# Kernel tuning notes

Measured on AMD Instinct MI355X. Metric: run time of the kernel, lower is better.

## Reference

```python
import jax, jax.numpy as jnp
import numpy as np
from jax import lax

GAMMA = 5.0
BETA = -2.5
EPS_EDGE = 1e-6
EPS_STD = 1e-6


def _fixed_kernels():
    """Stack 3 Sobel-x, 3 Sobel-y and Laplacian kernels, zero-padded to 7x7.
    Zero-padding a kernel symmetrically + padding=3 conv is mathematically
    identical to the per-scale padding=scale//2 convs in the original.
    Channel order: gx3, gy3, gx5, gy5, gx7, gy7, lap."""
    s3 = np.array([[-1, 0, 1], [-2, 0, 2], [-1, 0, 1]], np.float32)
    s5 = np.array([[-1, -2, 0, 2, 1], [-4, -8, 0, 8, 4], [-6, -12, 0, 12, 6],
                   [-4, -8, 0, 8, 4], [-1, -2, 0, 2, 1]], np.float32)
    s7 = np.array([[-1, -4, -5, 0, 5, 4, 1], [-6, -24, -30, 0, 30, 24, 6],
                   [-15, -60, -75, 0, 75, 60, 15], [-20, -80, -100, 0, 100, 80, 20],
                   [-15, -60, -75, 0, 75, 60, 15], [-6, -24, -30, 0, 30, 24, 6],
                   [-1, -4, -5, 0, 5, 4, 1]], np.float32)
    lap = np.array([[0, 1, 0], [1, -4, 1], [0, 1, 0]], np.float32)
    ks = []
    for k in (s3, s3.T, s5, s5.T, s7, s7.T, lap):
        p = (7 - k.shape[0]) // 2
        ks.append(np.pad(k, p))
    return jnp.asarray(np.stack(ks)[:, None])  # [7,1,7,7] OIHW


_KERNELS = _fixed_kernels()


def setup_inputs() -> dict:
    key = jax.random.key(0)
    x = jax.random.normal(key, (16, 64, 256, 256), dtype=jnp.float32)
    return {"x": x}


def reference(x):
    # grayscale: mean over channels -> [B,1,H,W]
    x_gray = x.mean(axis=1, keepdims=True)
    # single grouped conv producing all 7 filtered maps: [B,7,H,W]
    g = lax.conv_general_dilated(
        x_gray, _KERNELS.astype(x.dtype), window_strides=(1, 1),
        padding=((3, 3), (3, 3)),
        dimension_numbers=("NCHW", "OIHW", "NCHW"))
    gx = g[:, 0:6:2]  # [B,3,H,W]
    gy = g[:, 1:6:2]  # [B,3,H,W]
    edges = jnp.sqrt(gx * gx + gy * gy + EPS_EDGE)      # [B,3,H,W]
    lap_edge = jnp.abs(g[:, 6:7])                        # [B,1,H,W]
    # mean over the 4 concatenated edge channels
    combined = (edges.sum(axis=1, keepdims=True) + lap_edge) / 4.0  # [B,1,H,W]
    # per-image normalization (torch .std is unbiased -> ddof=1)
    mu = combined.mean(axis=(2, 3), keepdims=True)
    sigma = jnp.std(combined, axis=(2, 3), keepdims=True, ddof=1) + EPS_STD
    normalized = (combined - mu) / sigma
    boundary_map = jax.nn.sigmoid(GAMMA * normalized + BETA)
    return x * (1.0 + boundary_map)
```

## Files before the change

kernel.cpp:

```cpp
#include <hip/hip_runtime.h>
#include <math.h>

#define N_IMG 16
#define CCH   64
#define H     256
#define W     256
#define HW    (H*W)
#define HW4   (HW/4)
#define TS    16

typedef float fx4 __attribute__((ext_vector_type(4)));

__global__ __launch_bounds__(256) void gray_kernel(const float4* __restrict__ x,
                                                   float4* __restrict__ gray) {
    int bid = blockIdx.x;
    int n   = bid >> 6;
    int p4  = ((bid & 63) << 8) + threadIdx.x;
    const float4* xp = x + (size_t)n * CCH * HW4 + p4;
    float4 a0 = make_float4(0.f, 0.f, 0.f, 0.f);
    float4 a1 = a0, a2 = a0, a3 = a0;
    #pragma unroll
    for (int c = 0; c < CCH; c += 4) {
        float4 v0 = xp[(size_t)(c + 0) * HW4];
        float4 v1 = xp[(size_t)(c + 1) * HW4];
        float4 v2 = xp[(size_t)(c + 2) * HW4];
        float4 v3 = xp[(size_t)(c + 3) * HW4];
        a0.x += v0.x; a0.y += v0.y; a0.z += v0.z; a0.w += v0.w;
        a1.x += v1.x; a1.y += v1.y; a1.z += v1.z; a1.w += v1.w;
        a2.x += v2.x; a2.y += v2.y; a2.z += v2.z; a2.w += v2.w;
        a3.x += v3.x; a3.y += v3.y; a3.z += v3.z; a3.w += v3.w;
    }
    const float s = 1.0f / 64.0f;
    float4 acc;
    acc.x = (a0.x + a1.x + a2.x + a3.x) * s;
    acc.y = (a0.y + a1.y + a2.y + a3.y) * s;
    acc.z = (a0.z + a1.z + a2.z + a3.z) * s;
    acc.w = (a0.w + a1.w + a2.w + a3.w) * s;
    gray[(size_t)n * HW4 + p4] = acc;
}

__global__ __launch_bounds__(256) void conv_kernel(const float* __restrict__ gray,
                                                   float* __restrict__ comb,
                                                   float2* __restrict__ part) {
    __shared__ float t[TS + 6][TS + 7];
    __shared__ float rs[256];
    __shared__ float rq[256];
    int n  = blockIdx.z;
    int h0 = blockIdx.y * TS - 3;
    int w0 = blockIdx.x * TS - 3;
    const float* g = gray + (size_t)n * HW;

    int tid = threadIdx.y * TS + threadIdx.x;
    for (int i = tid; i < 22 * 22; i += 256) {
        int r  = i / 22, c2 = i - r * 22;
        int hh = h0 + r, ww = w0 + c2;
        t[r][c2] = (hh >= 0 && hh < H && ww >= 0 && ww < W) ? g[hh * W + ww] : 0.f;
    }
    __syncthreads();

    int ty = threadIdx.y, tx = threadIdx.x;
    float v[7][7];
    #pragma unroll
    for (int i = 0; i < 7; ++i)
        #pragma unroll
        for (int j = 0; j < 7; ++j)
            v[i][j] = t[ty + i][tx + j];

    float gx7 = 0.f, gy7 = 0.f;
    {
        const float vw[7] = {1.f, 6.f, 15.f, 20.f, 15.f, 6.f, 1.f};
        const float dw[7] = {-1.f, -4.f, -5.f, 0.f, 5.f, 4.f, 1.f};
        #pragma unroll
        for (int i = 0; i < 7; ++i) {
            float rh  = -v[i][0] - 4.f*v[i][1] - 5.f*v[i][2] + 5.f*v[i][4] + 4.f*v[i][5] + v[i][6];
            float rsu =  v[i][0] + 6.f*v[i][1] + 15.f*v[i][2] + 20.f*v[i][3] + 15.f*v[i][4] + 6.f*v[i][5] + v[i][6];
            gx7 += vw[i] * rh;
            gy7 += dw[i] * rsu;
        }
    }
    float gx5 = 0.f, gy5 = 0.f;
    {
        const float vw[5] = {1.f, 4.f, 6.f, 4.f, 1.f};
        const float dw[5] = {-1.f, -2.f, 0.f, 2.f, 1.f};
        #pragma unroll
        for (int i = 0; i < 5; ++i) {
            float rh  = -v[i+1][1] - 2.f*v[i+1][2] + 2.f*v[i+1][4] + v[i+1][5];
            float rsu =  v[i+1][1] + 4.f*v[i+1][2] + 6.f*v[i+1][3] + 4.f*v[i+1][4] + v[i+1][5];
            gx5 += vw[i] * rh;
            gy5 += dw[i] * rsu;
        }
    }
    float gx3 = 0.f, gy3 = 0.f;
    {
        const float vw[3] = {1.f, 2.f, 1.f};
        const float dw[3] = {-1.f, 0.f, 1.f};
        #pragma unroll
        for (int i = 0; i < 3; ++i) {
            float rh  = v[i+2][4] - v[i+2][2];
            float rsu = v[i+2][2] + 2.f*v[i+2][3] + v[i+2][4];
            gx3 += vw[i] * rh;
            gy3 += dw[i] * rsu;
        }
    }
    float lap = v[2][3] + v[4][3] + v[3][2] + v[3][4] - 4.f*v[3][3];

    float e3 = sqrtf(gx3*gx3 + gy3*gy3 + 1e-6f);
    float e5 = sqrtf(gx5*gx5 + gy5*gy5 + 1e-6f);
    float e7 = sqrtf(gx7*gx7 + gy7*gy7 + 1e-6f);
    float combined = (e3 + e5 + e7 + fabsf(lap)) * 0.25f;

    comb[(size_t)n * HW + (size_t)(h0 + 3 + ty) * W + (w0 + 3 + tx)] = combined;

    rs[tid] = combined;
    rq[tid] = combined * combined;
    __syncthreads();
    for (int off = 128; off > 0; off >>= 1) {
        if (tid < off) {
            rs[tid] += rs[tid + off];
            rq[tid] += rq[tid + off];
        }
        __syncthreads();
    }
    if (tid == 0) {
        int blockLin = blockIdx.y * (W / TS) + blockIdx.x;
        part[n * 256 + blockLin] = make_float2(rs[0], rq[0]);
    }
}

__global__ __launch_bounds__(256) void mul_kernel(const float4* __restrict__ x,
                                                  const float4* __restrict__ comb4,
                                                  const float2* __restrict__ part,
                                                  fx4* __restrict__ out) {
    __shared__ float rs[256];
    __shared__ float rq[256];
    int bid  = blockIdx.x;
    int n    = bid >> 7;
    int rest = bid & 127;
    int half = rest >> 6;
    int p4   = ((rest & 63) << 8) + threadIdx.x;
    int tid  = threadIdx.x;

    float2 p = part[n * 256 + tid];
    rs[tid] = p.x;
    rq[tid] = p.y;
    __syncthreads();
    for (int off = 128; off > 0; off >>= 1) {
        if (tid < off) {
            rs[tid] += rs[tid + off];
            rq[tid] += rq[tid + off];
        }
        __syncthreads();
    }
    float mu  = rs[0] / (float)HW;
    float var = (rq[0] - (float)HW * mu * mu) / (float)(HW - 1);
    var = fmaxf(var, 0.f);
    float inv = 1.0f / (sqrtf(var) + 1e-6f);

    float4 c = comb4[((size_t)n << 14) + p4];
    fx4 f;
    f.x = 1.0f + 1.0f / (1.0f + __expf(2.5f - 5.0f * (c.x - mu) * inv));
    f.y = 1.0f + 1.0f / (1.0f + __expf(2.5f - 5.0f * (c.y - mu) * inv));
    f.z = 1.0f + 1.0f / (1.0f + __expf(2.5f - 5.0f * (c.z - mu) * inv));
    f.w = 1.0f + 1.0f / (1.0f + __expf(2.5f - 5.0f * (c.w - mu) * inv));

    const int ch0 = half * 32;
    const float4* xp = x   + (size_t)n * CCH * HW4 + (size_t)ch0 * HW4 + p4;
    fx4*          op = out + (size_t)n * CCH * HW4 + (size_t)ch0 * HW4 + p4;
    #pragma unroll 8
    for (int ch = 0; ch < 32; ++ch) {
        float4 v = xp[(size_t)ch * HW4];
        fx4 r;
        r.x = v.x * f.x;
        r.y = v.y * f.y;
        r.z = v.z * f.z;
        r.w = v.w * f.w;
        __builtin_nontemporal_store(r, &op[(size_t)ch * HW4]);
    }
}

extern "C" void kernel_launch(void* const* d_in, const int* in_sizes, int n_in,
                              void* d_out, int out_size, void* d_ws, size_t ws_size,
                              hipStream_t stream) {
    const float* x = (const float*)d_in[0];
    float* out = (float*)d_out;
    char* ws = (char*)d_ws;

    float*  gray  = (float*)ws;
    float*  comb  = (float*)(ws + (size_t)N_IMG * HW * 4);
    float2* part  = (float2*)(ws + (size_t)2 * N_IMG * HW * 4);

    gray_kernel<<<N_IMG * 64, 256, 0, stream>>>((const float4*)x, (float4*)gray);

    dim3 cgrid(W / TS, H / TS, N_IMG);
    conv_kernel<<<cgrid, dim3(TS, TS), 0, stream>>>(gray, comb, part);

    mul_kernel<<<N_IMG * 128, 256, 0, stream>>>((const float4*)x, (const float4*)comb,
                                                part, (fx4*)out);
}
```

Baseline: 142.0 us.

## Finalize per-image stats in last conv block; split mul into quarter-channel blocks

```diff
diff --git a/kernel.cpp b/kernel.cpp
--- a/kernel.cpp
+++ b/kernel.cpp
@@ -41,10 +41,13 @@
 
 __global__ __launch_bounds__(256) void conv_kernel(const float* __restrict__ gray,
                                                    float* __restrict__ comb,
-                                                   float2* __restrict__ part) {
+                                                   float2* __restrict__ part,
+                                                   float2* __restrict__ stats,
+                                                   unsigned* __restrict__ cnt) {
     __shared__ float t[TS + 6][TS + 7];
     __shared__ float rs[256];
     __shared__ float rq[256];
+    __shared__ int sIsLast;
     int n  = blockIdx.z;
     int h0 = blockIdx.y * TS - 3;
     int w0 = blockIdx.x * TS - 3;
@@ -124,37 +127,45 @@
     if (tid == 0) {
         int blockLin = blockIdx.y * (W / TS) + blockIdx.x;
         part[n * 256 + blockLin] = make_float2(rs[0], rq[0]);
-    }
-}
-
-__global__ __launch_bounds__(256) void mul_kernel(const float4* __restrict__ x,
+        __threadfence();
+        unsigned old = atomicAdd(&cnt[n], 1u);
+        sIsLast = (old == 255u);
+    }
+    __syncthreads();
+
+    if (sIsLast) {
+        __threadfence();
+        float2 p = part[n * 256 + tid];
+        rs[tid] = p.x;
+        rq[tid] = p.y;
+        __syncthreads();
+        for (int off = 128; off > 0; off >>= 1) {
+            if (tid < off) {
+                rs[tid] += rs[tid + off];
+                rq[tid] += rq[tid + off];
+            }
+            __syncthreads();
+        }
+        if (tid == 0) {
+            float mu  = rs[0] / (float)HW;
+            float var = (rq[0] - (float)HW * mu * mu) / (float)(HW - 1);
+            var = fmaxf(var, 0.f);
+            stats[n] = make_float2(mu, 1.0f / (sqrtf(var) + 1e-6f));
+        }
+    }
+}
+
+__global__ __launch_bounds__(256) void mul_kernel(const fx4* __restrict__ x,
                                                   const float4* __restrict__ comb4,
-                                                  const float2* __restrict__ part,
+                                                  const float2* __restrict__ stats,
                                                   fx4* __restrict__ out) {
-    __shared__ float rs[256];
-    __shared__ float rq[256];
-    int bid  = blockIdx.x;
-    int n    = bid >> 7;
-    int rest = bid & 127;
-    int half = rest >> 6;
-    int p4   = ((rest & 63) << 8) + threadIdx.x;
-    int tid  = threadIdx.x;
-
-    float2 p = part[n * 256 + tid];
-    rs[tid] = p.x;
-    rq[tid] = p.y;
-    __syncthreads();
-    for (int off = 128; off > 0; off >>= 1) {
-        if (tid < off) {
-            rs[tid] += rs[tid + off];
-            rq[tid] += rq[tid + off];
-        }
-        __syncthreads();
-    }
-    float mu  = rs[0] / (float)HW;
-    float var = (rq[0] - (float)HW * mu * mu) / (float)(HW - 1);
-    var = fmaxf(var, 0.f);
-    float inv = 1.0f / (sqrtf(var) + 1e-6f);
+    int bid = blockIdx.x;
+    int n   = bid >> 8;
+    int q   = (bid >> 6) & 3;
+    int p4  = ((bid & 63) << 8) + threadIdx.x;
+
+    float2 st = stats[n];
+    float mu = st.x, inv = st.y;
 
     float4 c = comb4[((size_t)n << 14) + p4];
     fx4 f;
@@ -163,17 +174,13 @@
     f.z = 1.0f + 1.0f / (1.0f + __expf(2.5f - 5.0f * (c.z - mu) * inv));
     f.w = 1.0f + 1.0f / (1.0f + __expf(2.5f - 5.0f * (c.w - mu) * inv));
 
-    const int ch0 = half * 32;
-    const float4* xp = x   + (size_t)n * CCH * HW4 + (size_t)ch0 * HW4 + p4;
-    fx4*          op = out + (size_t)n * CCH * HW4 + (size_t)ch0 * HW4 + p4;
-    #pragma unroll 8
-    for (int ch = 0; ch < 32; ++ch) {
-        float4 v = xp[(size_t)ch * HW4];
-        fx4 r;
-        r.x = v.x * f.x;
-        r.y = v.y * f.y;
-        r.z = v.z * f.z;
-        r.w = v.w * f.w;
+    const int ch0 = q * 16;
+    const fx4* xp = x   + (size_t)n * CCH * HW4 + (size_t)ch0 * HW4 + p4;
+    fx4*       op = out + (size_t)n * CCH * HW4 + (size_t)ch0 * HW4 + p4;
+    #pragma unroll
+    for (int ch = 0; ch < 16; ++ch) {
+        fx4 v = __builtin_nontemporal_load(&xp[(size_t)ch * HW4]);
+        fx4 r = v * f;
         __builtin_nontemporal_store(r, &op[(size_t)ch * HW4]);
     }
 }
@@ -185,15 +192,19 @@
     float* out = (float*)d_out;
     char* ws = (char*)d_ws;
 
-    float*  gray  = (float*)ws;
-    float*  comb  = (float*)(ws + (size_t)N_IMG * HW * 4);
-    float2* part  = (float2*)(ws + (size_t)2 * N_IMG * HW * 4);
+    float*    gray  = (float*)ws;
+    float*    comb  = (float*)(ws + (size_t)N_IMG * HW * 4);
+    float2*   part  = (float2*)(ws + (size_t)2 * N_IMG * HW * 4);
+    float2*   stats = (float2*)((char*)part + 4096 * sizeof(float2));
+    unsigned* cnt   = (unsigned*)((char*)stats + N_IMG * sizeof(float2));
+
+    hipMemsetAsync(cnt, 0, N_IMG * sizeof(unsigned), stream);
 
     gray_kernel<<<N_IMG * 64, 256, 0, stream>>>((const float4*)x, (float4*)gray);
 
     dim3 cgrid(W / TS, H / TS, N_IMG);
-    conv_kernel<<<cgrid, dim3(TS, TS), 0, stream>>>(gray, comb, part);
-
-    mul_kernel<<<N_IMG * 128, 256, 0, stream>>>((const float4*)x, (const float4*)comb,
-                                                part, (fx4*)out);
-}
+    conv_kernel<<<cgrid, dim3(TS, TS), 0, stream>>>(gray, comb, part, stats, cnt);
+
+    mul_kernel<<<N_IMG * 256, 256, 0, stream>>>((const fx4*)x, (const float4*)comb,
+                                                stats, (fx4*)out);
+}
```

Result: slower. 256.3 us (+80.5%).
